# Optimization experiments

Hardware: AMD Instinct MI355X
Metric: run time of the kernel (lower is better)

The kernel has to match this reference:

```python
import jax, jax.numpy as jnp
import numpy as np

N_HEAD = 16
COND_LEN = 256  # n_unmasked; mask[i, j] == 1 iff j < COND_LEN + i


def rotate_half(x):
    # interleaved pairs: (x0, x1, x2, x3, ...) -> (-x1, x0, -x3, x2, ...)
    x = x.reshape(x.shape[:-1] + (-1, 2))
    x1, x2 = x[..., 0], x[..., 1]
    return jnp.stack([-x2, x1], axis=-1).reshape(x.shape[:-2] + (-1,))


def apply_rotary_pos_emb(t, freqs):
    # t: [B, H, T, l], freqs: [T, l] -> broadcast over B, H
    return t * jnp.cos(freqs) + rotate_half(t) * jnp.sin(freqs)


def setup_inputs() -> dict:
    key = jax.random.key(0)
    ks = jax.random.split(key, 12)
    B, T, C = 8, 769, 1024
    l = 32
    s = 0.02
    return {
        "x_q": jax.random.normal(ks[0], (B, T, C), jnp.float32),
        "x_kv": jax.random.normal(ks[1], (B, T, C), jnp.float32),
        "rotary_pos_emb": jax.random.uniform(ks[2], (T, l), jnp.float32),
        "Wq": jax.random.normal(ks[3], (C, C), jnp.float32) * s,
        "bq": jnp.zeros((C,), jnp.float32),
        "Wk": jax.random.normal(ks[4], (C, C), jnp.float32) * s,
        "bk": jnp.zeros((C,), jnp.float32),
        "Wv": jax.random.normal(ks[5], (C, C), jnp.float32) * s,
        "bv": jnp.zeros((C,), jnp.float32),
        "Wp": jax.random.normal(ks[6], (C, C), jnp.float32) * s,
        "bp": jnp.zeros((C,), jnp.float32),
    }


def reference(x_q, x_kv, rotary_pos_emb, Wq, bq, Wk, bk, Wv, bv, Wp, bp):
    B, T_q, C = x_q.shape
    T_kv = x_kv.shape[1]
    H = N_HEAD
    hd = C // H

    def heads(x, W, b, T):
        return (x @ W.T + b).reshape(B, T, H, hd).transpose(0, 2, 1, 3)  # [B,H,T,hd]

    q = heads(x_q, Wq, bq, T_q)
    k = heads(x_kv, Wk, bk, T_kv)
    v = heads(x_kv, Wv, bv, T_kv)

    # partial rotary on first l dims of q and k
    l = rotary_pos_emb.shape[-1]
    q = jnp.concatenate([apply_rotary_pos_emb(q[..., :l], rotary_pos_emb), q[..., l:]], axis=-1)
    k = jnp.concatenate([apply_rotary_pos_emb(k[..., :l], rotary_pos_emb), k[..., l:]], axis=-1)

    att = jnp.einsum("bhqd,bhkd->bhqk", q, k) * (1.0 / jnp.sqrt(jnp.asarray(hd, q.dtype)))
    # custom prefix+causal mask: allowed iff col < COND_LEN + row
    row = jnp.arange(T_q)[:, None]
    col = jnp.arange(T_kv)[None, :]
    allowed = col < (COND_LEN + row)  # [T_q, T_kv]
    att = jnp.where(allowed[None, None], att, -jnp.inf)
    att = jax.nn.softmax(att, axis=-1)

    y = jnp.einsum("bhqk,bhkd->bhqd", att, v)
    y = y.transpose(0, 2, 1, 3).reshape(B, T_q, C)
    return y @ Wp.T + bp
```

## Files before the change

### kernel.cpp

```cpp
#include <hip/hip_runtime.h>
#include <stdint.h>

#define B_    8
#define T_    769
#define C_    1024
#define H_    16
#define COND_ 256
#define NTOK  (B_*T_)
#define BH_   (B_*H_)
#define TP_   896

typedef short    v8s  __attribute__((ext_vector_type(8)));
typedef float    v4f  __attribute__((ext_vector_type(4)));
typedef uint16_t u16x4 __attribute__((ext_vector_type(4)));
typedef uint16_t u16x8 __attribute__((ext_vector_type(8)));

__device__ __forceinline__ uint16_t f2bf(float f) {
  uint32_t u = __builtin_bit_cast(uint32_t, f);
  u += 0x7fffu + ((u >> 16) & 1u);
  return (uint16_t)(u >> 16);
}
__device__ __forceinline__ float bf2f(uint16_t h) {
  uint32_t u = ((uint32_t)h) << 16;
  return __builtin_bit_cast(float, u);
}

__device__ __forceinline__ void gl_lds16(const void* gptr, void* lptr) {
  __builtin_amdgcn_global_load_lds(
      (const __attribute__((address_space(1))) uint32_t*)gptr,
      (__attribute__((address_space(3))) uint32_t*)lptr,
      16, 0, 0);
}

__device__ __forceinline__ int xcd_swz_bij(int orig, int nwg) {
  int q = nwg >> 3, r = nwg & 7;
  int xcd = orig & 7;
  int base = (xcd < r) ? xcd * (q + 1) : r * (q + 1) + (xcd - r) * q;
  return base + (orig >> 3);
}

__global__ __launch_bounds__(256) void convert_bf16(
    const float* xq, const float* xkv, const float* wq, const float* wk,
    const float* wv, const float* wp,
    uint16_t* dxq, uint16_t* dxkv, uint16_t* dwq, uint16_t* dwk,
    uint16_t* dwv, uint16_t* dwp)
{
  int bid = blockIdx.x;
  const float* s; uint16_t* d; int base;
  if (bid < 6152)       { s = xq;  d = dxq;  base = bid; }
  else if (bid < 12304) { s = xkv; d = dxkv; base = bid - 6152; }
  else {
    int r = bid - 12304;
    int wsel = r >> 10; base = r & 1023;
    s = (wsel == 0) ? wq : (wsel == 1) ? wk : (wsel == 2) ? wv : wp;
    d = (wsel == 0) ? dwq : (wsel == 1) ? dwk : (wsel == 2) ? dwv : dwp;
  }
  int i = base * 256 + threadIdx.x;
  float4 f = ((const float4*)s)[i];
  u16x4 o;
  o[0] = f2bf(f.x); o[1] = f2bf(f.y); o[2] = f2bf(f.z); o[3] = f2bf(f.w);
  ((u16x4*)d)[i] = o;
}


__global__ __launch_bounds__(256) void gemm_qkv(
    const uint16_t* xq, const uint16_t* xkv, const uint16_t* Wqkv,
    const float* bq, const float* bk, const float* bv, const float* freqs,
    uint16_t* Q, uint16_t* K, uint16_t* V)
{
  __shared__ uint16_t sA[2][4096];
  __shared__ uint16_t sB[2][4096];

  const int tid = threadIdx.x;
  const int lane = tid & 63, w = tid >> 6, quad = lane >> 4, l15 = lane & 15;
  const int rbase = (w >> 1) * 64, cbase = (w & 1) * 64;

  const int swz = xcd_swz_bij(blockIdx.x, 1176);
  const int ct = swz % 24, rt = swz / 24;
  const int z = ct >> 3;
  const int col0 = ct * 128, row0 = rt * 128;
  const uint16_t* A = (z == 0) ? xq : xkv;
  const float* bias  = (z == 0) ? bq : (z == 1 ? bk : bv);
  uint16_t* dst      = (z == 0) ? Q  : (z == 1 ? K  : V);

  const uint16_t* Ap[2];
  const uint16_t* Bp[2];
  #pragma unroll
  for (int r = 0; r < 2; r++) {
    int Cc = r * 256 + tid;
    int sr = Cc >> 3, sc = (Cc & 7) ^ (sr & 7);
    int row = sr * 2 + (sc >> 2), kc = sc & 3;
    Ap[r] = A    + (size_t)min(row0 + row, NTOK - 1) * 1024 + kc * 8;
    Bp[r] = Wqkv + (size_t)(col0 + row) * 1024 + kc * 8;
  }

  int offA[4], offB[4];
  #pragma unroll
  for (int i = 0; i < 4; i++) {
    int m = rbase + i * 16 + l15;
    int s0 = m >> 1;
    offA[i] = s0 * 64 + (((((m & 1) << 2) | quad) ^ (s0 & 7)) * 8);
    int n = cbase + i * 16 + l15;
    int sn = n >> 1;
    offB[i] = sn * 64 + (((((n & 1) << 2) | quad) ^ (sn & 7)) * 8);
  }

  v4f acc[4][4];
  #pragma unroll
  for (int i = 0; i < 4; i++)
    #pragma unroll
    for (int j = 0; j < 4; j++) acc[i][j] = (v4f)0.0f;

  #pragma unroll
  for (int r = 0; r < 2; r++) {
    gl_lds16(Ap[r] + 0,  sA[0] + (r * 256 + tid) * 8);
    gl_lds16(Bp[r] + 0,  sB[0] + (r * 256 + tid) * 8);
  }
  #pragma unroll
  for (int r = 0; r < 2; r++) {
    gl_lds16(Ap[r] + 32, sA[1] + (r * 256 + tid) * 8);
    gl_lds16(Bp[r] + 32, sB[1] + (r * 256 + tid) * 8);
  }

  #pragma unroll 1
  for (int t = 0; t < 32; t++) {
    if (t < 31) {
      asm volatile("s_waitcnt vmcnt(4)" ::: "memory");
    } else {
      asm volatile("s_waitcnt vmcnt(0)" ::: "memory");
    }
    __builtin_amdgcn_s_barrier();
    asm volatile("" ::: "memory");
    const uint16_t* cA = (t & 1) ? sA[1] : sA[0];
    const uint16_t* cB = (t & 1) ? sB[1] : sB[0];
    v8s af[4], bf[4];
    #pragma unroll
    for (int i = 0; i < 4; i++) af[i] = *(const v8s*)(cA + offA[i]);
    #pragma unroll
    for (int j = 0; j < 4; j++) bf[j] = *(const v8s*)(cB + offB[j]);
    asm volatile("s_waitcnt lgkmcnt(0)" ::: "memory");
    __builtin_amdgcn_s_barrier();
    asm volatile("" ::: "memory");
    if (t + 2 < 32) {
      uint16_t* nA = (t & 1) ? sA[1] : sA[0];
      uint16_t* nB = (t & 1) ? sB[1] : sB[0];
      int k0 = (t + 2) * 32;
      #pragma unroll
      for (int r = 0; r < 2; r++) {
        gl_lds16(Ap[r] + k0, nA + (r * 256 + tid) * 8);
        gl_lds16(Bp[r] + k0, nB + (r * 256 + tid) * 8);
      }
    }
    #pragma unroll
    for (int i = 0; i < 4; i++)
      #pragma unroll
      for (int j = 0; j < 4; j++)
        acc[i][j] = __builtin_amdgcn_mfma_f32_16x16x32_bf16(af[i], bf[j], acc[i][j], 0, 0, 0);
  }

  #pragma unroll
  for (int i = 0; i < 4; i++) {
    #pragma unroll
    for (int reg = 0; reg < 4; reg++) {
      int n = row0 + rbase + i * 16 + quad * 4 + reg;
      bool ok = (n < NTOK);
      int nn = min(n, NTOK - 1);
      int b = nn / T_, t = nn % T_;
      float vj[4];
      #pragma unroll
      for (int j = 0; j < 4; j++)
        vj[j] = acc[i][j][reg] + bias[(col0 + cbase + j * 16 + l15) & 1023];
      if (z < 2) {
        float v0 = vj[0], v1 = vj[1];
        float p0 = __shfl_xor(v0, 1);
        float p1 = __shfl_xor(v1, 1);
        float f0 = freqs[t * 32 + l15];
        float f1 = freqs[t * 32 + 16 + l15];
        float s0, c0, s1, c1;
        __sincosf(f0, &s0, &c0);
        __sincosf(f1, &s1, &c1);
        if (l15 & 1) { vj[0] = v0 * c0 + p0 * s0; vj[1] = v1 * c1 + p1 * s1; }
        else         { vj[0] = v0 * c0 - p0 * s0; vj[1] = v1 * c1 - p1 * s1; }
      }
      if (z == 0) {
        #pragma unroll
        for (int j = 0; j < 4; j++) vj[j] *= 0.125f;
      }
      if (ok) {
        #pragma unroll
        for (int j = 0; j < 4; j++) {
          int col = col0 + cbase + j * 16 + l15;
          int h = (col >> 6) & 15, d = col & 63;
          dst[((size_t)(b * H_ + h) * T_ + t) * 64 + d] = f2bf(vj[j]);
        }
      }
    }
  }
}

__device__ __forceinline__ void gemm_stage64(
    const uint16_t* const Aptr[4], const uint16_t* const Bptr[4],
    int k0, uint16_t* sA, uint16_t* sB, int tid)
{
  #pragma unroll
  for (int r = 0; r < 4; r++) {
    gl_lds16(Aptr[r] + k0, sA + (r * 256 + tid) * 8);
    gl_lds16(Bptr[r] + k0, sB + (r * 256 + tid) * 8);
  }
}

__device__ __forceinline__ void gemm_compute64(
    const uint16_t* sAc, const uint16_t* sBc, v4f acc[4][4],
    int rbase, int cbase, int quad, int l15)
{
  #pragma unroll
  for (int s = 0; s < 2; s++) {
    v8s af[4], bfv[4];
    #pragma unroll
    for (int i = 0; i < 4; i++) {
      int m = rbase + i * 16 + l15;
      af[i] = *(const v8s*)(sAc + m * 64 + (((s * 4 + quad) ^ (m & 7)) * 8));
    }
    #pragma unroll
    for (int j = 0; j < 4; j++) {
      int n = cbase + j * 16 + l15;
      bfv[j] = *(const v8s*)(sBc + n * 64 + (((s * 4 + quad) ^ (n & 7)) * 8));
    }
    #pragma unroll
    for (int i = 0; i < 4; i++)
      #pragma unroll
      for (int j = 0; j < 4; j++)
        acc[i][j] = __builtin_amdgcn_mfma_f32_16x16x32_bf16(af[i], bfv[j], acc[i][j], 0, 0, 0);
  }
}

__device__ __forceinline__ void gemm_mainloop64(
    const uint16_t* A, const uint16_t* W, int M, int row0, int col0,
    v4f acc[4][4], uint16_t* sA, uint16_t* sB)
{
  const int tid = threadIdx.x;
  const int lane = tid & 63, w = tid >> 6, quad = lane >> 4, l15 = lane & 15;
  const int rbase = (w >> 1) * 64, cbase = (w & 1) * 64;

  const uint16_t* Aptr[4];
  const uint16_t* Bptr[4];
  #pragma unroll
  for (int r = 0; r < 4; r++) {
    int c = r * 256 + tid;
    int row = c >> 3, qp = c & 7;
    int g = qp ^ (row & 7);
    Aptr[r] = A + (size_t)min(row0 + row, M - 1) * 1024 + g * 8;
    Bptr[r] = W + (size_t)(col0 + row) * 1024 + g * 8;
  }

  #pragma unroll
  for (int i = 0; i < 4; i++)
    #pragma unroll
    for (int j = 0; j < 4; j++) acc[i][j] = (v4f)0.0f;

  uint16_t* sA0 = sA;         uint16_t* sB0 = sB;
  uint16_t* sA1 = sA + 8192;  uint16_t* sB1 = sB + 8192;

  gemm_stage64(Aptr, Bptr, 0,  sA0, sB0, tid);
  gemm_stage64(Aptr, Bptr, 64, sA1, sB1, tid);

  #pragma unroll 1
  for (int t = 0; t < 16; t++) {
    if (t < 15) {
      asm volatile("s_waitcnt vmcnt(8)" ::: "memory");
    } else {
      asm volatile("s_waitcnt vmcnt(0)" ::: "memory");
    }
    __builtin_amdgcn_s_barrier();
    asm volatile("" ::: "memory");
    uint16_t* cA = (t & 1) ? sA1 : sA0;
    uint16_t* cB = (t & 1) ? sB1 : sB0;
    gemm_compute64(cA, cB, acc, rbase, cbase, quad, l15);
    asm volatile("s_waitcnt lgkmcnt(0)" ::: "memory");
    __builtin_amdgcn_s_barrier();
    asm volatile("" ::: "memory");
    if (t + 2 < 16)
      gemm_stage64(Aptr, Bptr, (t + 2) * 64, cA, cB, tid);
  }
}

__global__ __launch_bounds__(256) void gemm_out(
    const uint16_t* Y, const uint16_t* wp, const float* bp, float* out)
{
  __shared__ uint16_t sA[2 * 128 * 64];
  __shared__ uint16_t sB[2 * 128 * 64];
  const int swz = xcd_swz_bij(blockIdx.x, 392);
  const int ct = swz & 7, rt = swz >> 3;
  const int col0 = ct * 128, row0 = rt * 128;
  v4f acc[4][4];
  gemm_mainloop64(Y, wp, NTOK, row0, col0, acc, sA, sB);

  const int tid = threadIdx.x;
  const int lane = tid & 63, w = tid >> 6, quad = lane >> 4, l15 = lane & 15;
  const int rbase = (w >> 1) * 64, cbase = (w & 1) * 64;
  #pragma unroll
  for (int i = 0; i < 4; i++) {
    #pragma unroll
    for (int reg = 0; reg < 4; reg++) {
      int n = row0 + rbase + i * 16 + quad * 4 + reg;
      if (n < NTOK) {
        #pragma unroll
        for (int j = 0; j < 4; j++) {
          int col = col0 + cbase + j * 16 + l15;
          out[(size_t)n * 1024 + col] = acc[i][j][reg] + bp[col];
        }
      }
    }
  }
}

__global__ __launch_bounds__(256) void transpose_v(const uint16_t* Vb, uint16_t* Vt)
{
  __shared__ uint16_t sT[64 * 64];
  const int tid = threadIdx.x;
  const int t0 = blockIdx.x * 64, bh = blockIdx.y;
  const uint16_t* src = Vb + (size_t)bh * T_ * 64;
  #pragma unroll
  for (int r = 0; r < 2; r++) {
    int task = r * 256 + tid;
    int t = task >> 3, oc = task & 7;
    int gt = min(t0 + t, T_ - 1);
    u16x8 v = *(const u16x8*)(src + (size_t)gt * 64 + oc * 8);
    int p = oc ^ (t & 7) ^ ((t >> 3) & 7);
    *(u16x8*)(sT + t * 64 + p * 8) = v;
  }
  __syncthreads();
  uint16_t* dst = Vt + (size_t)bh * 64 * TP_;
  #pragma unroll
  for (int r = 0; r < 2; r++) {
    int task = r * 256 + tid;
    int o = task & 7, d = task >> 3;
    u16x8 v;
    #pragma unroll
    for (int k = 0; k < 8; k++) {
      int t = o * 8 + k;
      int p = (d >> 3) ^ k ^ o;
      v[k] = sT[t * 64 + p * 8 + (d & 7)];
    }
    *(u16x8*)(dst + (size_t)d * TP_ + t0 + o * 8) = v;
  }
}

__global__ __launch_bounds__(256) void attn(
    const uint16_t* Q, const uint16_t* K, const uint16_t* Vt, uint16_t* Y)
{
  __shared__ uint16_t sK[128 * 64];
  __shared__ uint16_t sVT[64 * 128];
  __shared__ uint16_t sP[4 * 16 * 136];

  const int tid = threadIdx.x;
  const int lane = tid & 63, w = tid >> 6, quad = lane >> 4, l15 = lane & 15;
  const int swz = xcd_swz_bij(blockIdx.x, 1664);
  const int qt = swz % 13, bh = swz / 13;
  const int b = bh >> 4, h = bh & 15;
  const int q0 = qt * 64;

  const uint16_t* Qb = Q + (size_t)bh * T_ * 64;
  const uint16_t* Kb = K + (size_t)bh * T_ * 64;
  const uint16_t* Vtb = Vt + (size_t)bh * 64 * TP_;

  const int qr = min(q0 + w * 16 + l15, T_ - 1);
  v8s aq0 = *(const v8s*)(Qb + (size_t)qr * 64 + quad * 8);
  v8s aq1 = *(const v8s*)(Qb + (size_t)qr * 64 + 32 + quad * 8);

  float l_r[4] = {0.f, 0.f, 0.f, 0.f};
  v4f o[4];
  #pragma unroll
  for (int r = 0; r < 4; r++) o[r] = (v4f)0.0f;

  const int kend = min(T_, q0 + 319);
  const int nkt = (kend + 127) >> 7;

  for (int kt = 0; kt < nkt; kt++) {
    const int k0 = kt * 128;
    #pragma unroll
    for (int r = 0; r < 4; r++) {
      int c = r * 256 + tid;
      int key = c >> 3, qp = c & 7;
      int g = qp ^ (key & 7);
      int gk = min(k0 + key, T_ - 1);
      gl_lds16(Kb + (size_t)gk * 64 + g * 8, sK + c * 8);
    }
    #pragma unroll
    for (int r = 0; r < 4; r++) {
      int c = r * 256 + tid;
      int d = c >> 4, p = c & 15;
      int g = (p & 8) | ((p ^ d) & 7);
      gl_lds16(Vtb + (size_t)d * TP_ + k0 + g * 8, sVT + c * 8);
    }
    __syncthreads();

    v4f s[8];
    #pragma unroll
    for (int cb = 0; cb < 8; cb++) {
      int key_l = cb * 16 + l15;
      v8s b0 = *(const v8s*)(sK + (key_l * 8 + ((quad) ^ (key_l & 7))) * 8);
      v8s b1 = *(const v8s*)(sK + (key_l * 8 + ((4 + quad) ^ (key_l & 7))) * 8);
      v4f zz = (v4f)0.0f;
      zz = __builtin_amdgcn_mfma_f32_16x16x32_bf16(aq0, b0, zz, 0, 0, 0);
      zz = __builtin_amdgcn_mfma_f32_16x16x32_bf16(aq1, b1, zz, 0, 0, 0);
      s[cb] = zz;
    }

    uint16_t* pw = sP + w * (16 * 136);
    const int qrow_base = q0 + w * 16 + quad * 4;
    const bool full = (k0 + 128 <= COND_ + q0) && (k0 + 128 <= T_);
    if (full) {
      #pragma unroll
      for (int reg = 0; reg < 4; reg++) {
        float rs = 0.f;
        #pragma unroll
        for (int cb = 0; cb < 8; cb++) {
          float pv = __expf(s[cb][reg]);
          uint16_t pb = f2bf(pv);
          rs += bf2f(pb);
          pw[(quad * 4 + reg) * 136 + cb * 16 + l15] = pb;
        }
        #pragma unroll
        for (int off = 1; off < 16; off <<= 1) rs += __shfl_xor(rs, off);
        l_r[reg] += rs;
      }
    } else {
      #pragma unroll
      for (int reg = 0; reg < 4; reg++) {
        int lim = min(COND_ + qrow_base + reg, T_);
        float rs = 0.f;
        #pragma unroll
        for (int cb = 0; cb < 8; cb++) {
          int key = k0 + cb * 16 + l15;
          float pv = (key < lim) ? __expf(s[cb][reg]) : 0.f;
          uint16_t pb = f2bf(pv);
          rs += bf2f(pb);
          pw[(quad * 4 + reg) * 136 + cb * 16 + l15] = pb;
        }
        #pragma unroll
        for (int off = 1; off < 16; off <<= 1) rs += __shfl_xor(rs, off);
        l_r[reg] += rs;
      }
    }

    #pragma unroll
    for (int ks = 0; ks < 4; ks++) {
      v8s ap = *(const v8s*)(pw + l15 * 136 + ks * 32 + quad * 8);
      #pragma unroll
      for (int cbd = 0; cbd < 4; cbd++) {
        int d = cbd * 16 + l15;
        v8s bv = *(const v8s*)(sVT + d * 128 + (((ks * 4 + quad) ^ (d & 7)) * 8));
        o[cbd] = __builtin_amdgcn_mfma_f32_16x16x32_bf16(ap, bv, o[cbd], 0, 0, 0);
      }
    }
    __syncthreads();
  }

  #pragma unroll
  for (int reg = 0; reg < 4; reg++) {
    int t = q0 + w * 16 + quad * 4 + reg;
    if (t < T_) {
      float inv = 1.0f / l_r[reg];
      #pragma unroll
      for (int cbd = 0; cbd < 4; cbd++) {
        int d = cbd * 16 + l15;
        Y[((size_t)(b * T_ + t)) * C_ + h * 64 + d] = f2bf(o[cbd][reg] * inv);
      }
    }
  }
}

extern "C" void kernel_launch(void* const* d_in, const int* in_sizes, int n_in,
                              void* d_out, int out_size, void* d_ws, size_t ws_size,
                              hipStream_t stream)
{
  const float* x_q   = (const float*)d_in[0];
  const float* x_kv  = (const float*)d_in[1];
  const float* freqs = (const float*)d_in[2];
  const float* Wq = (const float*)d_in[3];
  const float* bq = (const float*)d_in[4];
  const float* Wk = (const float*)d_in[5];
  const float* bk = (const float*)d_in[6];
  const float* Wv = (const float*)d_in[7];
  const float* bv = (const float*)d_in[8];
  const float* Wp = (const float*)d_in[9];
  const float* bp = (const float*)d_in[10];
  float* out = (float*)d_out;

  const size_t SZX = (size_t)NTOK * C_;
  const size_t SZW = (size_t)C_ * C_;
  uint16_t* ws = (uint16_t*)d_ws;
  uint16_t* xq_bf  = ws;
  uint16_t* xkv_bf = xq_bf + SZX;
  uint16_t* wq_bf  = xkv_bf + SZX;
  uint16_t* wk_bf  = wq_bf + SZW;
  uint16_t* wv_bf  = wk_bf + SZW;
  uint16_t* wp_bf  = wv_bf + SZW;
  uint16_t* Qb = wp_bf + SZW;
  uint16_t* Kb = Qb + SZX;
  uint16_t* Vb = Kb + SZX;
  uint16_t* Vt = ws;
  uint16_t* Yb = Vb;

  convert_bf16<<<dim3(16400), 256, 0, stream>>>(
      x_q, x_kv, Wq, Wk, Wv, Wp, xq_bf, xkv_bf, wq_bf, wk_bf, wv_bf, wp_bf);

  gemm_qkv<<<dim3(1176), 256, 0, stream>>>(
      xq_bf, xkv_bf, wq_bf, bq, bk, bv, freqs, Qb, Kb, Vb);

  transpose_v<<<dim3(13, BH_), 256, 0, stream>>>(Vb, Vt);

  attn<<<dim3(1664), 256, 0, stream>>>(Qb, Kb, Vt, Yb);

  gemm_out<<<dim3(392), 256, 0, stream>>>(Yb, wp_bf, bp, out);
}
```

Baseline: 267.1 us.

## Use 128-row attention tiles with 8 waves and a K=32 out-projection pipeline

```diff
diff --git a/kernel.cpp b/kernel.cpp
--- a/kernel.cpp
+++ b/kernel.cpp
@@ -62,7 +62,6 @@
   ((u16x4*)d)[i] = o;
 }
 
-
 __global__ __launch_bounds__(256) void gemm_qkv(
     const uint16_t* xq, const uint16_t* xkv, const uint16_t* Wqkv,
     const float* bq, const float* bk, const float* bv, const float* freqs,
@@ -198,106 +197,95 @@
   }
 }
 
-__device__ __forceinline__ void gemm_stage64(
-    const uint16_t* const Aptr[4], const uint16_t* const Bptr[4],
-    int k0, uint16_t* sA, uint16_t* sB, int tid)
+__global__ __launch_bounds__(256) void gemm_out(
+    const uint16_t* Y, const uint16_t* wp, const float* bp, float* out)
 {
-  #pragma unroll
-  for (int r = 0; r < 4; r++) {
-    gl_lds16(Aptr[r] + k0, sA + (r * 256 + tid) * 8);
-    gl_lds16(Bptr[r] + k0, sB + (r * 256 + tid) * 8);
-  }
-}
-
-__device__ __forceinline__ void gemm_compute64(
-    const uint16_t* sAc, const uint16_t* sBc, v4f acc[4][4],
-    int rbase, int cbase, int quad, int l15)
-{
-  #pragma unroll
-  for (int s = 0; s < 2; s++) {
-    v8s af[4], bfv[4];
-    #pragma unroll
-    for (int i = 0; i < 4; i++) {
-      int m = rbase + i * 16 + l15;
-      af[i] = *(const v8s*)(sAc + m * 64 + (((s * 4 + quad) ^ (m & 7)) * 8));
-    }
-    #pragma unroll
-    for (int j = 0; j < 4; j++) {
-      int n = cbase + j * 16 + l15;
-      bfv[j] = *(const v8s*)(sBc + n * 64 + (((s * 4 + quad) ^ (n & 7)) * 8));
-    }
-    #pragma unroll
-    for (int i = 0; i < 4; i++)
-      #pragma unroll
-      for (int j = 0; j < 4; j++)
-        acc[i][j] = __builtin_amdgcn_mfma_f32_16x16x32_bf16(af[i], bfv[j], acc[i][j], 0, 0, 0);
-  }
-}
-
-__device__ __forceinline__ void gemm_mainloop64(
-    const uint16_t* A, const uint16_t* W, int M, int row0, int col0,
-    v4f acc[4][4], uint16_t* sA, uint16_t* sB)
-{
+  __shared__ uint16_t sA[2][4096];
+  __shared__ uint16_t sB[2][4096];
+
   const int tid = threadIdx.x;
   const int lane = tid & 63, w = tid >> 6, quad = lane >> 4, l15 = lane & 15;
   const int rbase = (w >> 1) * 64, cbase = (w & 1) * 64;
 
-  const uint16_t* Aptr[4];
-  const uint16_t* Bptr[4];
-  #pragma unroll
-  for (int r = 0; r < 4; r++) {
-    int c = r * 256 + tid;
-    int row = c >> 3, qp = c & 7;
-    int g = qp ^ (row & 7);
-    Aptr[r] = A + (size_t)min(row0 + row, M - 1) * 1024 + g * 8;
-    Bptr[r] = W + (size_t)(col0 + row) * 1024 + g * 8;
-  }
-
+  const int swz = xcd_swz_bij(blockIdx.x, 392);
+  const int ct = swz & 7, rt = swz >> 3;
+  const int col0 = ct * 128, row0 = rt * 128;
+
+  const uint16_t* Ap[2];
+  const uint16_t* Bp[2];
+  #pragma unroll
+  for (int r = 0; r < 2; r++) {
+    int Cc = r * 256 + tid;
+    int sr = Cc >> 3, sc = (Cc & 7) ^ (sr & 7);
+    int row = sr * 2 + (sc >> 2), kc = sc & 3;
+    Ap[r] = Y  + (size_t)min(row0 + row, NTOK - 1) * 1024 + kc * 8;
+    Bp[r] = wp + (size_t)(col0 + row) * 1024 + kc * 8;
+  }
+
+  int offA[4], offB[4];
+  #pragma unroll
+  for (int i = 0; i < 4; i++) {
+    int m = rbase + i * 16 + l15;
+    int s0 = m >> 1;
+    offA[i] = s0 * 64 + (((((m & 1) << 2) | quad) ^ (s0 & 7)) * 8);
+    int n = cbase + i * 16 + l15;
+    int sn = n >> 1;
+    offB[i] = sn * 64 + (((((n & 1) << 2) | quad) ^ (sn & 7)) * 8);
+  }
+
+  v4f acc[4][4];
   #pragma unroll
   for (int i = 0; i < 4; i++)
     #pragma unroll
     for (int j = 0; j < 4; j++) acc[i][j] = (v4f)0.0f;
 
-  uint16_t* sA0 = sA;         uint16_t* sB0 = sB;
-  uint16_t* sA1 = sA + 8192;  uint16_t* sB1 = sB + 8192;
-
-  gemm_stage64(Aptr, Bptr, 0,  sA0, sB0, tid);
-  gemm_stage64(Aptr, Bptr, 64, sA1, sB1, tid);
+  #pragma unroll
+  for (int r = 0; r < 2; r++) {
+    gl_lds16(Ap[r] + 0,  sA[0] + (r * 256 + tid) * 8);
+    gl_lds16(Bp[r] + 0,  sB[0] + (r * 256 + tid) * 8);
+  }
+  #pragma unroll
+  for (int r = 0; r < 2; r++) {
+    gl_lds16(Ap[r] + 32, sA[1] + (r * 256 + tid) * 8);
+    gl_lds16(Bp[r] + 32, sB[1] + (r * 256 + tid) * 8);
+  }
 
   #pragma unroll 1
-  for (int t = 0; t < 16; t++) {
-    if (t < 15) {
-      asm volatile("s_waitcnt vmcnt(8)" ::: "memory");
+  for (int t = 0; t < 32; t++) {
+    if (t < 31) {
+      asm volatile("s_waitcnt vmcnt(4)" ::: "memory");
     } else {
       asm volatile("s_waitcnt vmcnt(0)" ::: "memory");
     }
     __builtin_amdgcn_s_barrier();
     asm volatile("" ::: "memory");
-    uint16_t* cA = (t & 1) ? sA1 : sA0;
-    uint16_t* cB = (t & 1) ? sB1 : sB0;
-    gemm_compute64(cA, cB, acc, rbase, cbase, quad, l15);
+    const uint16_t* cA = (t & 1) ? sA[1] : sA[0];
+    const uint16_t* cB = (t & 1) ? sB[1] : sB[0];
+    v8s af[4], bf[4];
+    #pragma unroll
+    for (int i = 0; i < 4; i++) af[i] = *(const v8s*)(cA + offA[i]);
+    #pragma unroll
+    for (int j = 0; j < 4; j++) bf[j] = *(const v8s*)(cB + offB[j]);
     asm volatile("s_waitcnt lgkmcnt(0)" ::: "memory");
     __builtin_amdgcn_s_barrier();
     asm volatile("" ::: "memory");
-    if (t + 2 < 16)
-      gemm_stage64(Aptr, Bptr, (t + 2) * 64, cA, cB, tid);
-  }
-}
-
-__global__ __launch_bounds__(256) void gemm_out(
-    const uint16_t* Y, const uint16_t* wp, const float* bp, float* out)
-{
-  __shared__ uint16_t sA[2 * 128 * 64];
-  __shared__ uint16_t sB[2 * 128 * 64];
-  const int swz = xcd_swz_bij(blockIdx.x, 392);
-  const int ct = swz & 7, rt = swz >> 3;
-  const int col0 = ct * 128, row0 = rt * 128;
-  v4f acc[4][4];
-  gemm_mainloop64(Y, wp, NTOK, row0, col0, acc, sA, sB);
-
-  const int tid = threadIdx.x;
-  const int lane = tid & 63, w = tid >> 6, quad = lane >> 4, l15 = lane & 15;
-  const int rbase = (w >> 1) * 64, cbase = (w & 1) * 64;
+    if (t + 2 < 32) {
+      uint16_t* nA = (t & 1) ? sA[1] : sA[0];
+      uint16_t* nB = (t & 1) ? sB[1] : sB[0];
+      int k0 = (t + 2) * 32;
+      #pragma unroll
+      for (int r = 0; r < 2; r++) {
+        gl_lds16(Ap[r] + k0, nA + (r * 256 + tid) * 8);
+        gl_lds16(Bp[r] + k0, nB + (r * 256 + tid) * 8);
+      }
+    }
+    #pragma unroll
+    for (int i = 0; i < 4; i++)
+      #pragma unroll
+      for (int j = 0; j < 4; j++)
+        acc[i][j] = __builtin_amdgcn_mfma_f32_16x16x32_bf16(af[i], bf[j], acc[i][j], 0, 0, 0);
+  }
+
   #pragma unroll
   for (int i = 0; i < 4; i++) {
     #pragma unroll
@@ -346,19 +334,19 @@
   }
 }
 
-__global__ __launch_bounds__(256) void attn(
+__global__ __launch_bounds__(512) void attn(
     const uint16_t* Q, const uint16_t* K, const uint16_t* Vt, uint16_t* Y)
 {
   __shared__ uint16_t sK[128 * 64];
   __shared__ uint16_t sVT[64 * 128];
-  __shared__ uint16_t sP[4 * 16 * 136];
+  __shared__ uint16_t sP[8 * 16 * 136];
 
   const int tid = threadIdx.x;
   const int lane = tid & 63, w = tid >> 6, quad = lane >> 4, l15 = lane & 15;
-  const int swz = xcd_swz_bij(blockIdx.x, 1664);
-  const int qt = swz % 13, bh = swz / 13;
+  const int swz = xcd_swz_bij(blockIdx.x, 896);
+  const int qt = swz % 7, bh = swz / 7;
   const int b = bh >> 4, h = bh & 15;
-  const int q0 = qt * 64;
+  const int q0 = qt * 128;
 
   const uint16_t* Qb = Q + (size_t)bh * T_ * 64;
   const uint16_t* Kb = K + (size_t)bh * T_ * 64;
@@ -373,22 +361,22 @@
   #pragma unroll
   for (int r = 0; r < 4; r++) o[r] = (v4f)0.0f;
 
-  const int kend = min(T_, q0 + 319);
+  const int kend = min(T_, q0 + 383);
   const int nkt = (kend + 127) >> 7;
 
   for (int kt = 0; kt < nkt; kt++) {
     const int k0 = kt * 128;
     #pragma unroll
-    for (int r = 0; r < 4; r++) {
-      int c = r * 256 + tid;
+    for (int r = 0; r < 2; r++) {
+      int c = r * 512 + tid;
       int key = c >> 3, qp = c & 7;
       int g = qp ^ (key & 7);
       int gk = min(k0 + key, T_ - 1);
       gl_lds16(Kb + (size_t)gk * 64 + g * 8, sK + c * 8);
     }
     #pragma unroll
-    for (int r = 0; r < 4; r++) {
-      int c = r * 256 + tid;
+    for (int r = 0; r < 2; r++) {
+      int c = r * 512 + tid;
       int d = c >> 4, p = c & 15;
       int g = (p & 8) | ((p ^ d) & 7);
       gl_lds16(Vtb + (size_t)d * TP_ + k0 + g * 8, sVT + c * 8);
@@ -511,7 +499,7 @@
 
   transpose_v<<<dim3(13, BH_), 256, 0, stream>>>(Vb, Vt);
 
-  attn<<<dim3(1664), 256, 0, stream>>>(Qb, Kb, Vt, Yb);
+  attn<<<dim3(896), 512, 0, stream>>>(Qb, Kb, Vt, Yb);
 
   gemm_out<<<dim3(392), 256, 0, stream>>>(Yb, wp_bf, bp, out);
 }
```

After: 282.5 us. +5.7%, slower.
